# Kernel optimization log

Measured on AMD Instinct MI355X. Metric: run time of the kernel, lower is better.

The kernel has to match this reference:

```python
import jax, jax.numpy as jnp
import numpy as np

D = 128          # node_state_dim
N_NODES = 5000
WINDOW = 10
N_TOTAL = WINDOW * N_NODES
E = 131072       # structural (int) edges
T = 2            # message passing steps
HID = 1024


def setup_inputs() -> dict:
    key = jax.random.key(0)
    ks = jax.random.split(key, 20)
    ie = jax.random.randint(ks[0], (E, 3), 0, N_NODES, dtype=jnp.int32)
    int_edges = jnp.stack([ie[:, 0] % WINDOW, ie[:, 1], ie[:, 2]], axis=1)
    nodes = jax.random.randint(ks[1], (N_NODES,), 0, 10, dtype=jnp.int32)

    def init(k, shape, scale=0.05):
        return (jax.random.normal(k, shape, jnp.float32) * scale)

    params = dict(
        embed_table=init(ks[2], (10, D)),
        msg_W1=init(ks[3], (2 * D, HID)), msg_b1=jnp.zeros((HID,), jnp.float32),
        msg_W2=init(ks[4], (HID, D)), msg_b2=jnp.zeros((D,), jnp.float32),
        gru_int_W=init(ks[5], (D, 3 * D)), gru_int_U=init(ks[6], (D, 3 * D)),
        gru_int_b=jnp.zeros((2, 3 * D), jnp.float32),
        gru_temp_W=init(ks[7], (D, 3 * D)), gru_temp_U=init(ks[8], (D, 3 * D)),
        gru_temp_b=jnp.zeros((2, 3 * D), jnp.float32),
        ro_W1=init(ks[9], (D, HID)), ro_b1=jnp.zeros((HID,), jnp.float32),
        ro_W2=init(ks[10], (HID, 512)), ro_b2=jnp.zeros((512,), jnp.float32),
        ro_W3=init(ks[11], (512, 10)), ro_b3=jnp.zeros((10,), jnp.float32),
    )
    return {"int_edges": int_edges, "nodes": nodes, **params}


def _temp_edges():
    fwd_src = np.arange(0, N_TOTAL - N_NODES)
    fwd_dst = fwd_src + N_NODES
    bwd_src = np.arange(N_NODES, N_TOTAL)
    bwd_dst = bwd_src - N_NODES
    src = jnp.asarray(np.concatenate([fwd_src, bwd_src]), jnp.int32)
    dst = jnp.asarray(np.concatenate([fwd_dst, bwd_dst]), jnp.int32)
    return src, dst


def _gru(x, h, W, U, b):
    # Keras GRUCell, reset_after=True. x,h: [N,D]; W,U: [D,3D]; b: [2,3D]
    xg = x @ W + b[0]
    hg = h @ U + b[1]
    xz, xr, xh = jnp.split(xg, 3, axis=-1)
    hz, hr, hh = jnp.split(hg, 3, axis=-1)
    z = jax.nn.sigmoid(xz + hz)
    r = jax.nn.sigmoid(xr + hr)
    hcand = jnp.tanh(xh + r * hh)
    return z * h + (1.0 - z) * hcand


def _msg(x, W1, b1, W2, b2):
    # Dense(1024,relu) -> Dropout(inference: identity) -> Dense(D,relu)
    return jax.nn.relu(jax.nn.relu(x @ W1 + b1) @ W2 + b2)


def _seg_mean(x, idx, n):
    s = jax.ops.segment_sum(x, idx, num_segments=n)
    c = jax.ops.segment_sum(jnp.ones((x.shape[0],), x.dtype), idx, num_segments=n)
    return jnp.where(c[:, None] > 0, s / jnp.maximum(c, 1.0)[:, None], 0.0)


def reference(int_edges, nodes, embed_table, msg_W1, msg_b1, msg_W2, msg_b2,
              gru_int_W, gru_int_U, gru_int_b, gru_temp_W, gru_temp_U, gru_temp_b,
              ro_W1, ro_b1, ro_W2, ro_b2, ro_W3, ro_b3):
    node_idx = int_edges[:, 0] * N_NODES + int_edges[:, 1]        # [E]
    neigh_idx = int_edges[:, 0] * N_NODES + int_edges[:, 2]       # [E]
    t_src, t_dst = _temp_edges()

    h = embed_table[nodes]                                        # [n_nodes, D]
    h = jnp.repeat(h, WINDOW, axis=0)                             # [N_TOTAL, D]

    for _ in range(T):
        # structural edges
        m_in = jnp.concatenate([h[node_idx], h[neigh_idx]], axis=1)   # [E, 2D]
        m = _msg(m_in, msg_W1, msg_b1, msg_W2, msg_b2)                # [E, D]
        agg = _seg_mean(m, neigh_idx, N_TOTAL)                        # [N_TOTAL, D]
        h = _gru(agg, h, gru_int_W, gru_int_U, gru_int_b)
        # temporal edges
        tm_in = jnp.concatenate([h[t_src], h[t_dst]], axis=1)
        tm = _msg(tm_in, msg_W1, msg_b1, msg_W2, msg_b2)
        tagg = _seg_mean(tm, t_dst, N_TOTAL)
        h = _gru(tagg, h, gru_temp_W, gru_temp_U, gru_temp_b)

    # readout on first frame's nodes
    x = h[:N_NODES]
    x = jax.nn.relu(x @ ro_W1 + ro_b1)
    x = jax.nn.relu(x @ ro_W2 + ro_b2)
    return jax.nn.softmax(x @ ro_W3 + ro_b3, axis=-1)
```

## Files before the change

kernel.cpp:

```cpp
#include <hip/hip_runtime.h>
#include <math.h>

#define D 128
#define N_NODES 5000
#define WINDOW 10
#define N_TOTAL 50000
#define NE_INT 131072
#define NE_TMP 90000
#define NE_FWD (N_TOTAL - N_NODES)
#define HID 1024

typedef short bf16x8 __attribute__((ext_vector_type(8)));
typedef float f32x4 __attribute__((ext_vector_type(4)));

#define SA 264
#define SH 136
#define SK 136
#define SCAN_B 256

static __device__ __forceinline__ short f2bf(float f) {
    union { float f; unsigned u; } v; v.f = f;
    unsigned r = v.u + 0x7fffu + ((v.u >> 16) & 1u);
    return (short)(r >> 16);
}
static __device__ __forceinline__ float bf2f(short s) {
    union { unsigned u; float f; } v;
    v.u = ((unsigned)(unsigned short)s) << 16;
    return v.f;
}
static __device__ __forceinline__ float lo_bf(unsigned u) {
    union { unsigned u; float f; } v; v.u = u << 16; return v.f;
}
static __device__ __forceinline__ float hi_bf(unsigned u) {
    union { unsigned u; float f; } v; v.u = u & 0xffff0000u; return v.f;
}

struct TcvtArgs {
    const float* in[8];
    short* out[8];
    int K[8];
    int N[8];
};
__global__ void k_tcvt8(TcvtArgs a) {
    int i = blockIdx.x * blockDim.x + threadIdx.x;
#pragma unroll
    for (int s = 0; s < 8; ++s) {
        int sz = a.K[s] * a.N[s];
        if (i < sz) {
            int n = i / a.K[s], k = i - n * a.K[s];
            a.out[s][i] = f2bf(a.in[s][(size_t)k * a.N[s] + n]);
            return;
        }
        i -= sz;
    }
}

__global__ void k_init_h(const int* __restrict__ nodes, const float* __restrict__ embed,
                         float* __restrict__ h32, short* __restrict__ h16) {
    int i = blockIdx.x * blockDim.x + threadIdx.x;
    if (i >= N_TOTAL * D) return;
    int row = i >> 7;
    int c = i & 127;
    int n = nodes[row / WINDOW];
    float v = embed[n * D + c];
    h32[i] = v;
    h16[i] = f2bf(v);
}

__global__ void k_build_int_edges(const int* __restrict__ ie, int* __restrict__ src,
                                  int* __restrict__ dst, int* __restrict__ icnt) {
    int e = blockIdx.x * blockDim.x + threadIdx.x;
    if (e >= NE_INT) return;
    int t = ie[e * 3 + 0], a = ie[e * 3 + 1], b = ie[e * 3 + 2];
    int d = t * N_NODES + b;
    src[e] = t * N_NODES + a;
    dst[e] = d;
    atomicAdd(&icnt[d], 1);
}

__global__ void k_build_tmp_edges(int* __restrict__ src, int* __restrict__ dst) {
    int e = blockIdx.x * blockDim.x + threadIdx.x;
    if (e >= NE_TMP) return;
    int s, d;
    if (e < NE_FWD) { s = e; d = e + N_NODES; }
    else { int q = e - NE_FWD; s = q + N_NODES; d = q; }
    src[e] = s;
    dst[e] = d;
}

__global__ void k_scan_partial(const int* __restrict__ cnt, int* __restrict__ rowstart,
                               int* __restrict__ btot, int n) {
    __shared__ int s[SCAN_B];
    int tid = threadIdx.x;
    int i = blockIdx.x * SCAN_B + tid;
    int v = (i < n) ? cnt[i] : 0;
    s[tid] = v;
    __syncthreads();
    for (int off = 1; off < SCAN_B; off <<= 1) {
        int x = (tid >= off) ? s[tid - off] : 0;
        __syncthreads();
        s[tid] += x;
        __syncthreads();
    }
    if (i < n) rowstart[i] = s[tid] - v;
    if (tid == SCAN_B - 1) btot[blockIdx.x] = s[tid];
}

__global__ void k_scan_block(int* __restrict__ btot, int nb) {
    __shared__ int s[SCAN_B];
    int tid = threadIdx.x;
    int v = (tid < nb) ? btot[tid] : 0;
    s[tid] = v;
    __syncthreads();
    for (int off = 1; off < SCAN_B; off <<= 1) {
        int x = (tid >= off) ? s[tid - off] : 0;
        __syncthreads();
        s[tid] += x;
        __syncthreads();
    }
    if (tid < nb) btot[tid] = s[tid] - v;
}

__global__ void k_scan_add(int* __restrict__ rowstart, const int* __restrict__ btot,
                           int* __restrict__ cursor, int n, int total) {
    int i = blockIdx.x * blockDim.x + threadIdx.x;
    if (i < n) {
        int v = rowstart[i] + btot[i >> 8];
        rowstart[i] = v;
        cursor[i] = v;
    }
    if (i == 0) rowstart[n] = total;
}

__global__ void k_fill_csr(const int* __restrict__ dst, int nE, int* __restrict__ cursor,
                           int* __restrict__ pmap) {
    int e = blockIdx.x * blockDim.x + threadIdx.x;
    if (e >= nE) return;
    int p = atomicAdd(&cursor[dst[e]], 1);
    pmap[e] = p;
}

__global__ void __launch_bounds__(256, 1) k_msg_mfma(
    const short* __restrict__ h16, const int* __restrict__ src, const int* __restrict__ dst,
    const int* __restrict__ pmap, int nE,
    const short* __restrict__ W1T, const float* __restrict__ b1,
    const short* __restrict__ W2T, const float* __restrict__ b2,
    short* __restrict__ m)
{
    __shared__ short Ain[128 * SA];
    __shared__ short Hid[128 * SH];

    int t = threadIdx.x;
    int e0 = blockIdx.x * 128;

    {
        int r = t >> 1, q = t & 1;
        int e = e0 + r;
        int ec = (e < nE) ? e : (nE - 1);
        uint4* ao = (uint4*)(Ain + r * SA);
        if (q == 0) {
            const uint4* ps = (const uint4*)(h16 + (size_t)src[ec] * D);
#pragma unroll
            for (int i = 0; i < 16; ++i) ao[i] = ps[i];
        } else {
            const uint4* pd = (const uint4*)(h16 + (size_t)dst[ec] * D);
#pragma unroll
            for (int i = 0; i < 16; ++i) ao[16 + i] = pd[i];
        }
    }
    __syncthreads();

    int w = t >> 6, lane = t & 63;
    int lm = lane & 15, lk = lane >> 4;

    f32x4 c2[2][8];
#pragma unroll
    for (int cs = 0; cs < 2; ++cs) {
        int out0 = w * 32 + cs * 16 + lk * 4;
#pragma unroll
        for (int et = 0; et < 8; ++et)
#pragma unroll
            for (int rg = 0; rg < 4; ++rg) c2[cs][et][rg] = b2[out0 + rg];
    }

    for (int hc = 0; hc < 8; ++hc) {
        f32x4 c1[2][8];
#pragma unroll
        for (int cs = 0; cs < 2; ++cs) {
            int ch0 = hc * 128 + w * 32 + cs * 16 + lk * 4;
#pragma unroll
            for (int et = 0; et < 8; ++et)
#pragma unroll
                for (int rg = 0; rg < 4; ++rg) c1[cs][et][rg] = b1[ch0 + rg];
        }
#pragma unroll
        for (int kk = 0; kk < 8; ++kk) {
            int ko = kk * 32 + lk * 8;
            bf16x8 a0 = *(const bf16x8*)(W1T + (size_t)(hc * 128 + w * 32 + lm) * 256 + ko);
            bf16x8 a1 = *(const bf16x8*)(W1T + (size_t)(hc * 128 + w * 32 + 16 + lm) * 256 + ko);
            bf16x8 bf[8];
#pragma unroll
            for (int et = 0; et < 8; ++et)
                bf[et] = *(const bf16x8*)(Ain + (et * 16 + lm) * SA + ko);
#pragma unroll
            for (int et = 0; et < 8; ++et) {
                c1[0][et] = __builtin_amdgcn_mfma_f32_16x16x32_bf16(a0, bf[et], c1[0][et], 0, 0, 0);
                c1[1][et] = __builtin_amdgcn_mfma_f32_16x16x32_bf16(a1, bf[et], c1[1][et], 0, 0, 0);
            }
        }
        __syncthreads();
#pragma unroll
        for (int cs = 0; cs < 2; ++cs) {
            int ch_in = w * 32 + cs * 16 + lk * 4;
#pragma unroll
            for (int et = 0; et < 8; ++et) {
                int edge = et * 16 + lm;
                short4 sv;
                sv.x = f2bf(fmaxf(c1[cs][et][0], 0.f));
                sv.y = f2bf(fmaxf(c1[cs][et][1], 0.f));
                sv.z = f2bf(fmaxf(c1[cs][et][2], 0.f));
                sv.w = f2bf(fmaxf(c1[cs][et][3], 0.f));
                *(short4*)(Hid + edge * SH + ch_in) = sv;
            }
        }
        __syncthreads();

#pragma unroll
        for (int kk = 0; kk < 4; ++kk) {
            int ko = kk * 32 + lk * 8;
            bf16x8 a0 = *(const bf16x8*)(W2T + (size_t)(w * 32 + lm) * 1024 + hc * 128 + ko);
            bf16x8 a1 = *(const bf16x8*)(W2T + (size_t)(w * 32 + 16 + lm) * 1024 + hc * 128 + ko);
            bf16x8 bf[8];
#pragma unroll
            for (int et = 0; et < 8; ++et)
                bf[et] = *(const bf16x8*)(Hid + (et * 16 + lm) * SH + ko);
#pragma unroll
            for (int et = 0; et < 8; ++et) {
                c2[0][et] = __builtin_amdgcn_mfma_f32_16x16x32_bf16(a0, bf[et], c2[0][et], 0, 0, 0);
                c2[1][et] = __builtin_amdgcn_mfma_f32_16x16x32_bf16(a1, bf[et], c2[1][et], 0, 0, 0);
            }
        }
    }

#pragma unroll
    for (int et = 0; et < 8; ++et) {
        int edge = et * 16 + lm;
        int e = e0 + edge;
        if (e >= nE) continue;
        int slot = pmap ? pmap[e] : e;
        short* rowp = m + (size_t)slot * 128;
#pragma unroll
        for (int cs = 0; cs < 2; ++cs) {
            int out0 = w * 32 + cs * 16 + lk * 4;
            short4 sv;
            sv.x = f2bf(fmaxf(c2[cs][et][0], 0.f));
            sv.y = f2bf(fmaxf(c2[cs][et][1], 0.f));
            sv.z = f2bf(fmaxf(c2[cs][et][2], 0.f));
            sv.w = f2bf(fmaxf(c2[cs][et][3], 0.f));
            *(short4*)(rowp + out0) = sv;
        }
    }
}

__global__ void __launch_bounds__(256, 4) k_gru_mfma(
    const short* __restrict__ m, const int* __restrict__ rowstart, int mode,
    float* __restrict__ h32, short* __restrict__ h16,
    const short* __restrict__ WT, const short* __restrict__ UT,
    const float* __restrict__ b)
{
    __shared__ short Ax[64 * SK];
    __shared__ short Hx[64 * SK];
    int t = threadIdx.x;
    int r0 = blockIdx.x * 64;

    {
        int r = t >> 2, q = t & 3;
        int row = r0 + r;
        int rc = (row < N_TOTAL) ? row : (N_TOTAL - 1);
        const uint4* hp = (const uint4*)(h16 + (size_t)rc * D);
        uint4* hxo = (uint4*)(Hx + r * SK);
#pragma unroll
        for (int i = 0; i < 4; ++i) hxo[q * 4 + i] = hp[q * 4 + i];

        float acc[32];
#pragma unroll
        for (int i = 0; i < 32; ++i) acc[i] = 0.f;
        int deg = 0;
        if (row < N_TOTAL) {
            if (mode == 0) {
                int s0 = rowstart[row], s1 = rowstart[row + 1];
                deg = s1 - s0;
                for (int p = s0; p < s1; ++p) {
                    const uint4* mp = (const uint4*)(m + (size_t)p * 128 + q * 32);
#pragma unroll
                    for (int i = 0; i < 4; ++i) {
                        uint4 v = mp[i];
                        unsigned ua[4] = {v.x, v.y, v.z, v.w};
#pragma unroll
                        for (int j = 0; j < 4; ++j) {
                            acc[i * 8 + 2 * j]     += lo_bf(ua[j]);
                            acc[i * 8 + 2 * j + 1] += hi_bf(ua[j]);
                        }
                    }
                }
            } else {
                if (row >= N_NODES) {
                    const uint4* mp = (const uint4*)(m + (size_t)(row - N_NODES) * 128 + q * 32);
                    ++deg;
#pragma unroll
                    for (int i = 0; i < 4; ++i) {
                        uint4 v = mp[i];
                        unsigned ua[4] = {v.x, v.y, v.z, v.w};
#pragma unroll
                        for (int j = 0; j < 4; ++j) {
                            acc[i * 8 + 2 * j]     += lo_bf(ua[j]);
                            acc[i * 8 + 2 * j + 1] += hi_bf(ua[j]);
                        }
                    }
                }
                if (row < NE_FWD) {
                    const uint4* mp = (const uint4*)(m + (size_t)(NE_FWD + row) * 128 + q * 32);
                    ++deg;
#pragma unroll
                    for (int i = 0; i < 4; ++i) {
                        uint4 v = mp[i];
                        unsigned ua[4] = {v.x, v.y, v.z, v.w};
#pragma unroll
                        for (int j = 0; j < 4; ++j) {
                            acc[i * 8 + 2 * j]     += lo_bf(ua[j]);
                            acc[i * 8 + 2 * j + 1] += hi_bf(ua[j]);
                        }
                    }
                }
            }
        }
        float inv = (deg > 0) ? 1.f / (float)deg : 0.f;
        uint4* axp = (uint4*)(Ax + r * SK + q * 32);
#pragma unroll
        for (int i = 0; i < 4; ++i) {
            union { uint4 u; short s[8]; } pk;
#pragma unroll
            for (int j = 0; j < 8; ++j) pk.s[j] = f2bf(acc[i * 8 + j] * inv);
            axp[i] = pk.u;
        }
    }
    __syncthreads();

    int w = t >> 6, lane = t & 63;
    int lm = lane & 15, lk = lane >> 4;

    for (int g = 0; g < 8; ++g) {
        int ch = g * 16 + lm;
        f32x4 cxz, cxr, cxh, chz, chr_, chh;
#pragma unroll
        for (int rg = 0; rg < 4; ++rg) {
            cxz[rg] = b[ch];        chz[rg] = b[384 + ch];
            cxr[rg] = b[128 + ch];  chr_[rg] = b[384 + 128 + ch];
            cxh[rg] = b[256 + ch];  chh[rg] = b[384 + 256 + ch];
        }
#pragma unroll
        for (int kk = 0; kk < 4; ++kk) {
            int ko = kk * 32 + lk * 8;
            bf16x8 ax = *(const bf16x8*)(Ax + (w * 16 + lm) * SK + ko);
            bf16x8 hx = *(const bf16x8*)(Hx + (w * 16 + lm) * SK + ko);
            bf16x8 bz = *(const bf16x8*)(WT + (size_t)(ch) * 128 + ko);
            bf16x8 br = *(const bf16x8*)(WT + (size_t)(128 + ch) * 128 + ko);
            bf16x8 bh = *(const bf16x8*)(WT + (size_t)(256 + ch) * 128 + ko);
            bf16x8 uz = *(const bf16x8*)(UT + (size_t)(ch) * 128 + ko);
            bf16x8 ur = *(const bf16x8*)(UT + (size_t)(128 + ch) * 128 + ko);
            bf16x8 uh = *(const bf16x8*)(UT + (size_t)(256 + ch) * 128 + ko);
            cxz = __builtin_amdgcn_mfma_f32_16x16x32_bf16(ax, bz, cxz, 0, 0, 0);
            cxr = __builtin_amdgcn_mfma_f32_16x16x32_bf16(ax, br, cxr, 0, 0, 0);
            cxh = __builtin_amdgcn_mfma_f32_16x16x32_bf16(ax, bh, cxh, 0, 0, 0);
            chz = __builtin_amdgcn_mfma_f32_16x16x32_bf16(hx, uz, chz, 0, 0, 0);
            chr_ = __builtin_amdgcn_mfma_f32_16x16x32_bf16(hx, ur, chr_, 0, 0, 0);
            chh = __builtin_amdgcn_mfma_f32_16x16x32_bf16(hx, uh, chh, 0, 0, 0);
        }
#pragma unroll
        for (int rg = 0; rg < 4; ++rg) {
            int row = r0 + w * 16 + lk * 4 + rg;
            if (row >= N_TOTAL) continue;
            float z = 1.f / (1.f + expf(-(cxz[rg] + chz[rg])));
            float r_ = 1.f / (1.f + expf(-(cxr[rg] + chr_[rg])));
            float hcv = tanhf(cxh[rg] + r_ * chh[rg]);
            size_t idx = (size_t)row * D + ch;
            float hold = h32[idx];
            float hnew = z * hold + (1.f - z) * hcv;
            h32[idx] = hnew;
            h16[idx] = f2bf(hnew);
        }
    }
}

__global__ void __launch_bounds__(256, 4) k_ro_mfma(
    const short* __restrict__ A16, const short* __restrict__ BT,
    const float* __restrict__ bias, float* __restrict__ C32, short* __restrict__ C16,
    int M, int N, int K)
{
    __shared__ short As[64 * SK];
    int t = threadIdx.x;
    int mb = blockIdx.y * 64;
    int nb = blockIdx.x * 128;
    int w = t >> 6, lane = t & 63;
    int lm = lane & 15, lk = lane >> 4;

    f32x4 acc[8];
#pragma unroll
    for (int nt = 0; nt < 8; ++nt) {
        float bv = bias[nb + nt * 16 + lm];
        acc[nt][0] = bv; acc[nt][1] = bv; acc[nt][2] = bv; acc[nt][3] = bv;
    }

    for (int kc = 0; kc < K; kc += 128) {
        __syncthreads();
        {
            int r = t >> 2, q = t & 3;
            int row = mb + r;
            int rc = (row < M) ? row : (M - 1);
            const uint4* ap = (const uint4*)(A16 + (size_t)rc * K + kc);
            uint4* ao = (uint4*)(As + r * SK);
#pragma unroll
            for (int i = 0; i < 4; ++i) ao[i * 4 + q] = ap[i * 4 + q];
        }
        __syncthreads();
#pragma unroll
        for (int kk = 0; kk < 4; ++kk) {
            int ko = kk * 32 + lk * 8;
            bf16x8 a = *(const bf16x8*)(As + (w * 16 + lm) * SK + ko);
#pragma unroll
            for (int nt = 0; nt < 8; ++nt) {
                bf16x8 bfr = *(const bf16x8*)(BT + (size_t)(nb + nt * 16 + lm) * K + kc + ko);
                acc[nt] = __builtin_amdgcn_mfma_f32_16x16x32_bf16(a, bfr, acc[nt], 0, 0, 0);
            }
        }
    }
#pragma unroll
    for (int nt = 0; nt < 8; ++nt) {
        int col = nb + nt * 16 + lm;
#pragma unroll
        for (int rg = 0; rg < 4; ++rg) {
            int row = mb + w * 16 + lk * 4 + rg;
            if (row >= M) continue;
            float v = fmaxf(acc[nt][rg], 0.f);
            if (C32) C32[(size_t)row * N + col] = v;
            if (C16) C16[(size_t)row * N + col] = f2bf(v);
        }
    }
}

__global__ void __launch_bounds__(64) k_logits_softmax(
    const float* __restrict__ r2, const float* __restrict__ W3,
    const float* __restrict__ b3, float* __restrict__ out)
{
    int row = blockIdx.x;
    int t = threadIdx.x;
    float p[10];
#pragma unroll
    for (int j = 0; j < 10; ++j) p[j] = 0.f;
    for (int k = t; k < 512; k += 64) {
        float v = r2[(size_t)row * 512 + k];
#pragma unroll
        for (int j = 0; j < 10; ++j) p[j] += v * W3[k * 10 + j];
    }
#pragma unroll
    for (int j = 0; j < 10; ++j) {
        float s = p[j];
        for (int off = 32; off > 0; off >>= 1) s += __shfl_down(s, off);
        p[j] = s;
    }
    if (t == 0) {
        float mx = -1e30f;
#pragma unroll
        for (int j = 0; j < 10; ++j) { p[j] += b3[j]; mx = fmaxf(mx, p[j]); }
        float sum = 0.f;
#pragma unroll
        for (int j = 0; j < 10; ++j) { p[j] = expf(p[j] - mx); sum += p[j]; }
        float inv = 1.f / sum;
#pragma unroll
        for (int j = 0; j < 10; ++j) out[(size_t)row * 10 + j] = p[j] * inv;
    }
}

extern "C" void kernel_launch(void* const* d_in, const int* in_sizes, int n_in,
                              void* d_out, int out_size, void* d_ws, size_t ws_size,
                              hipStream_t stream)
{
    const int*   ie    = (const int*)d_in[0];
    const int*   nodes = (const int*)d_in[1];
    const float* embed = (const float*)d_in[2];
    const float* mW1   = (const float*)d_in[3];
    const float* mb1   = (const float*)d_in[4];
    const float* mW2   = (const float*)d_in[5];
    const float* mb2   = (const float*)d_in[6];
    const float* giW   = (const float*)d_in[7];
    const float* giU   = (const float*)d_in[8];
    const float* gib   = (const float*)d_in[9];
    const float* gtW   = (const float*)d_in[10];
    const float* gtU   = (const float*)d_in[11];
    const float* gtb   = (const float*)d_in[12];
    const float* rW1   = (const float*)d_in[13];
    const float* rb1   = (const float*)d_in[14];
    const float* rW2   = (const float*)d_in[15];
    const float* rb2   = (const float*)d_in[16];
    const float* rW3   = (const float*)d_in[17];
    const float* rb3   = (const float*)d_in[18];
    float* out = (float*)d_out;

    char* ws = (char*)d_ws;
    size_t off = 0;
    auto alloc = [&](size_t bytes) {
        void* p = ws + off;
        off += (bytes + 255) & ~(size_t)255;
        return p;
    };
    float* h32   = (float*)alloc((size_t)N_TOTAL * D * 4);
    short* h16   = (short*)alloc((size_t)N_TOTAL * D * 2);
    short* m     = (short*)alloc((size_t)NE_INT * 128 * 2);
    int*   icnt  = (int*)alloc((size_t)N_TOTAL * 4);
    int*   rowst = (int*)alloc((size_t)(N_TOTAL + 1) * 4);
    int*   btot  = (int*)alloc(256 * 4);
    int*   curs  = (int*)alloc((size_t)N_TOTAL * 4);
    int*   pmap  = (int*)alloc((size_t)NE_INT * 4);
    int*   srcA  = (int*)alloc((size_t)NE_INT * 4);
    int*   dstA  = (int*)alloc((size_t)NE_INT * 4);
    int*   srcT  = (int*)alloc((size_t)NE_TMP * 4);
    int*   dstT  = (int*)alloc((size_t)NE_TMP * 4);
    short* mW1T  = (short*)alloc((size_t)HID * 256 * 2);
    short* mW2T  = (short*)alloc((size_t)D * HID * 2);
    short* giWT  = (short*)alloc((size_t)384 * D * 2);
    short* giUT  = (short*)alloc((size_t)384 * D * 2);
    short* gtWT  = (short*)alloc((size_t)384 * D * 2);
    short* gtUT  = (short*)alloc((size_t)384 * D * 2);
    short* rW1T  = (short*)alloc((size_t)HID * D * 2);
    short* rW2T  = (short*)alloc((size_t)512 * HID * 2);
    short* r1_16 = (short*)alloc((size_t)N_NODES * HID * 2);
    float* r2_32 = (float*)alloc((size_t)N_NODES * 512 * 4);

    {
        TcvtArgs a;
        a.in[0] = mW1; a.out[0] = mW1T; a.K[0] = 256; a.N[0] = HID;
        a.in[1] = mW2; a.out[1] = mW2T; a.K[1] = HID; a.N[1] = D;
        a.in[2] = giW; a.out[2] = giWT; a.K[2] = D;   a.N[2] = 384;
        a.in[3] = giU; a.out[3] = giUT; a.K[3] = D;   a.N[3] = 384;
        a.in[4] = gtW; a.out[4] = gtWT; a.K[4] = D;   a.N[4] = 384;
        a.in[5] = gtU; a.out[5] = gtUT; a.K[5] = D;   a.N[5] = 384;
        a.in[6] = rW1; a.out[6] = rW1T; a.K[6] = D;   a.N[6] = HID;
        a.in[7] = rW2; a.out[7] = rW2T; a.K[7] = HID; a.N[7] = 512;
        int total = 256 * HID + HID * D + 4 * (D * 384) + D * HID + HID * 512;
        k_tcvt8<<<(total + 255) / 256, 256, 0, stream>>>(a);
    }

    hipMemsetAsync(icnt, 0, (size_t)N_TOTAL * 4, stream);
    k_init_h<<<(N_TOTAL * D + 255) / 256, 256, 0, stream>>>(nodes, embed, h32, h16);
    k_build_int_edges<<<(NE_INT + 255) / 256, 256, 0, stream>>>(ie, srcA, dstA, icnt);
    k_build_tmp_edges<<<(NE_TMP + 255) / 256, 256, 0, stream>>>(srcT, dstT);
    int nb = (N_TOTAL + SCAN_B - 1) / SCAN_B;
    k_scan_partial<<<nb, SCAN_B, 0, stream>>>(icnt, rowst, btot, N_TOTAL);
    k_scan_block<<<1, SCAN_B, 0, stream>>>(btot, nb);
    k_scan_add<<<nb, SCAN_B, 0, stream>>>(rowst, btot, curs, N_TOTAL, NE_INT);
    k_fill_csr<<<(NE_INT + 255) / 256, 256, 0, stream>>>(dstA, NE_INT, curs, pmap);

    int gmsgA = (NE_INT + 127) / 128;
    int gmsgT = (NE_TMP + 127) / 128;
    int ggru = (N_TOTAL + 63) / 64;
    for (int it = 0; it < 2; ++it) {
        k_msg_mfma<<<gmsgA, 256, 0, stream>>>(h16, srcA, dstA, pmap, NE_INT, mW1T, mb1, mW2T, mb2, m);
        k_gru_mfma<<<ggru, 256, 0, stream>>>(m, rowst, 0, h32, h16, giWT, giUT, gib);

        k_msg_mfma<<<gmsgT, 256, 0, stream>>>(h16, srcT, dstT, (const int*)nullptr, NE_TMP, mW1T, mb1, mW2T, mb2, m);
        k_gru_mfma<<<ggru, 256, 0, stream>>>(m, rowst, 1, h32, h16, gtWT, gtUT, gtb);
    }

    dim3 g1(HID / 128, (N_NODES + 63) / 64);
    k_ro_mfma<<<g1, 256, 0, stream>>>(h16, rW1T, rb1, (float*)nullptr, r1_16, N_NODES, HID, D);
    dim3 g2(512 / 128, (N_NODES + 63) / 64);
    k_ro_mfma<<<g2, 256, 0, stream>>>(r1_16, rW2T, rb2, r2_32, (short*)nullptr, N_NODES, 512, HID);
    k_logits_softmax<<<N_NODES, 64, 0, stream>>>(r2_32, rW3, rb3, out);
}
```

Measured before the change: 1.240 ms.

## Fuse segment-mean scatter into message kernel via fp32 atomics, drop CSR build

The message kernel now atomically adds each ReLU'd fp32 message into a per-node aggregation buffer indexed by destination. Previously it wrote bf16 messages into CSR slots and the GRU kernel gathered them. This removes the scan and CSR-fill kernels and the gather loop in the GRU, and avoids materializing per-edge messages. The cost is 128 fp32 atomics per edge, a memset of the 25.6MB aggregation buffer before each message pass, and summation order that is no longer deterministic.

```diff
diff --git a/kernel.cpp b/kernel.cpp
--- a/kernel.cpp
+++ b/kernel.cpp
@@ -16,7 +16,6 @@
 #define SA 264
 #define SH 136
 #define SK 136
-#define SCAN_B 256
 
 static __device__ __forceinline__ short f2bf(float f) {
     union { float f; unsigned u; } v; v.f = f;
@@ -27,12 +26,6 @@
     union { unsigned u; float f; } v;
     v.u = ((unsigned)(unsigned short)s) << 16;
     return v.f;
-}
-static __device__ __forceinline__ float lo_bf(unsigned u) {
-    union { unsigned u; float f; } v; v.u = u << 16; return v.f;
-}
-static __device__ __forceinline__ float hi_bf(unsigned u) {
-    union { unsigned u; float f; } v; v.u = u & 0xffff0000u; return v.f;
 }
 
 struct TcvtArgs {
@@ -88,64 +81,12 @@
     dst[e] = d;
 }
 
-__global__ void k_scan_partial(const int* __restrict__ cnt, int* __restrict__ rowstart,
-                               int* __restrict__ btot, int n) {
-    __shared__ int s[SCAN_B];
-    int tid = threadIdx.x;
-    int i = blockIdx.x * SCAN_B + tid;
-    int v = (i < n) ? cnt[i] : 0;
-    s[tid] = v;
-    __syncthreads();
-    for (int off = 1; off < SCAN_B; off <<= 1) {
-        int x = (tid >= off) ? s[tid - off] : 0;
-        __syncthreads();
-        s[tid] += x;
-        __syncthreads();
-    }
-    if (i < n) rowstart[i] = s[tid] - v;
-    if (tid == SCAN_B - 1) btot[blockIdx.x] = s[tid];
-}
-
-__global__ void k_scan_block(int* __restrict__ btot, int nb) {
-    __shared__ int s[SCAN_B];
-    int tid = threadIdx.x;
-    int v = (tid < nb) ? btot[tid] : 0;
-    s[tid] = v;
-    __syncthreads();
-    for (int off = 1; off < SCAN_B; off <<= 1) {
-        int x = (tid >= off) ? s[tid - off] : 0;
-        __syncthreads();
-        s[tid] += x;
-        __syncthreads();
-    }
-    if (tid < nb) btot[tid] = s[tid] - v;
-}
-
-__global__ void k_scan_add(int* __restrict__ rowstart, const int* __restrict__ btot,
-                           int* __restrict__ cursor, int n, int total) {
-    int i = blockIdx.x * blockDim.x + threadIdx.x;
-    if (i < n) {
-        int v = rowstart[i] + btot[i >> 8];
-        rowstart[i] = v;
-        cursor[i] = v;
-    }
-    if (i == 0) rowstart[n] = total;
-}
-
-__global__ void k_fill_csr(const int* __restrict__ dst, int nE, int* __restrict__ cursor,
-                           int* __restrict__ pmap) {
-    int e = blockIdx.x * blockDim.x + threadIdx.x;
-    if (e >= nE) return;
-    int p = atomicAdd(&cursor[dst[e]], 1);
-    pmap[e] = p;
-}
-
 __global__ void __launch_bounds__(256, 1) k_msg_mfma(
     const short* __restrict__ h16, const int* __restrict__ src, const int* __restrict__ dst,
-    const int* __restrict__ pmap, int nE,
+    int nE,
     const short* __restrict__ W1T, const float* __restrict__ b1,
     const short* __restrict__ W2T, const float* __restrict__ b2,
-    short* __restrict__ m)
+    float* __restrict__ agg)
 {
     __shared__ short Ain[128 * SA];
     __shared__ short Hid[128 * SH];
@@ -247,23 +188,20 @@
         int edge = et * 16 + lm;
         int e = e0 + edge;
         if (e >= nE) continue;
-        int slot = pmap ? pmap[e] : e;
-        short* rowp = m + (size_t)slot * 128;
+        int d = dst[e];
+        float* rowp = agg + (size_t)d * 128;
 #pragma unroll
         for (int cs = 0; cs < 2; ++cs) {
             int out0 = w * 32 + cs * 16 + lk * 4;
-            short4 sv;
-            sv.x = f2bf(fmaxf(c2[cs][et][0], 0.f));
-            sv.y = f2bf(fmaxf(c2[cs][et][1], 0.f));
-            sv.z = f2bf(fmaxf(c2[cs][et][2], 0.f));
-            sv.w = f2bf(fmaxf(c2[cs][et][3], 0.f));
-            *(short4*)(rowp + out0) = sv;
+#pragma unroll
+            for (int rg = 0; rg < 4; ++rg)
+                atomicAdd(rowp + out0 + rg, fmaxf(c2[cs][et][rg], 0.f));
         }
     }
 }
 
 __global__ void __launch_bounds__(256, 4) k_gru_mfma(
-    const short* __restrict__ m, const int* __restrict__ rowstart, int mode,
+    const float* __restrict__ agg, const int* __restrict__ icnt, int mode,
     float* __restrict__ h32, short* __restrict__ h16,
     const short* __restrict__ WT, const short* __restrict__ UT,
     const float* __restrict__ b)
@@ -282,65 +220,20 @@
 #pragma unroll
         for (int i = 0; i < 4; ++i) hxo[q * 4 + i] = hp[q * 4 + i];
 
-        float acc[32];
-#pragma unroll
-        for (int i = 0; i < 32; ++i) acc[i] = 0.f;
-        int deg = 0;
-        if (row < N_TOTAL) {
-            if (mode == 0) {
-                int s0 = rowstart[row], s1 = rowstart[row + 1];
-                deg = s1 - s0;
-                for (int p = s0; p < s1; ++p) {
-                    const uint4* mp = (const uint4*)(m + (size_t)p * 128 + q * 32);
-#pragma unroll
-                    for (int i = 0; i < 4; ++i) {
-                        uint4 v = mp[i];
-                        unsigned ua[4] = {v.x, v.y, v.z, v.w};
-#pragma unroll
-                        for (int j = 0; j < 4; ++j) {
-                            acc[i * 8 + 2 * j]     += lo_bf(ua[j]);
-                            acc[i * 8 + 2 * j + 1] += hi_bf(ua[j]);
-                        }
-                    }
-                }
-            } else {
-                if (row >= N_NODES) {
-                    const uint4* mp = (const uint4*)(m + (size_t)(row - N_NODES) * 128 + q * 32);
-                    ++deg;
-#pragma unroll
-                    for (int i = 0; i < 4; ++i) {
-                        uint4 v = mp[i];
-                        unsigned ua[4] = {v.x, v.y, v.z, v.w};
-#pragma unroll
-                        for (int j = 0; j < 4; ++j) {
-                            acc[i * 8 + 2 * j]     += lo_bf(ua[j]);
-                            acc[i * 8 + 2 * j + 1] += hi_bf(ua[j]);
-                        }
-                    }
-                }
-                if (row < NE_FWD) {
-                    const uint4* mp = (const uint4*)(m + (size_t)(NE_FWD + row) * 128 + q * 32);
-                    ++deg;
-#pragma unroll
-                    for (int i = 0; i < 4; ++i) {
-                        uint4 v = mp[i];
-                        unsigned ua[4] = {v.x, v.y, v.z, v.w};
-#pragma unroll
-                        for (int j = 0; j < 4; ++j) {
-                            acc[i * 8 + 2 * j]     += lo_bf(ua[j]);
-                            acc[i * 8 + 2 * j + 1] += hi_bf(ua[j]);
-                        }
-                    }
-                }
-            }
+        int deg;
+        if (mode == 0) {
+            deg = icnt[rc];
+        } else {
+            deg = (rc >= N_NODES ? 1 : 0) + (rc < NE_FWD ? 1 : 0);
         }
         float inv = (deg > 0) ? 1.f / (float)deg : 0.f;
+        const float* ap = agg + (size_t)rc * 128 + q * 32;
         uint4* axp = (uint4*)(Ax + r * SK + q * 32);
 #pragma unroll
         for (int i = 0; i < 4; ++i) {
             union { uint4 u; short s[8]; } pk;
 #pragma unroll
-            for (int j = 0; j < 8; ++j) pk.s[j] = f2bf(acc[i * 8 + j] * inv);
+            for (int j = 0; j < 8; ++j) pk.s[j] = f2bf(ap[i * 8 + j] * inv);
             axp[i] = pk.u;
         }
     }
@@ -515,12 +408,8 @@
     };
     float* h32   = (float*)alloc((size_t)N_TOTAL * D * 4);
     short* h16   = (short*)alloc((size_t)N_TOTAL * D * 2);
-    short* m     = (short*)alloc((size_t)NE_INT * 128 * 2);
+    float* agg   = (float*)alloc((size_t)N_TOTAL * D * 4);
     int*   icnt  = (int*)alloc((size_t)N_TOTAL * 4);
-    int*   rowst = (int*)alloc((size_t)(N_TOTAL + 1) * 4);
-    int*   btot  = (int*)alloc(256 * 4);
-    int*   curs  = (int*)alloc((size_t)N_TOTAL * 4);
-    int*   pmap  = (int*)alloc((size_t)NE_INT * 4);
     int*   srcA  = (int*)alloc((size_t)NE_INT * 4);
     int*   dstA  = (int*)alloc((size_t)NE_INT * 4);
     int*   srcT  = (int*)alloc((size_t)NE_TMP * 4);
@@ -554,21 +443,19 @@
     k_init_h<<<(N_TOTAL * D + 255) / 256, 256, 0, stream>>>(nodes, embed, h32, h16);
     k_build_int_edges<<<(NE_INT + 255) / 256, 256, 0, stream>>>(ie, srcA, dstA, icnt);
     k_build_tmp_edges<<<(NE_TMP + 255) / 256, 256, 0, stream>>>(srcT, dstT);
-    int nb = (N_TOTAL + SCAN_B - 1) / SCAN_B;
-    k_scan_partial<<<nb, SCAN_B, 0, stream>>>(icnt, rowst, btot, N_TOTAL);
-    k_scan_block<<<1, SCAN_B, 0, stream>>>(btot, nb);
-    k_scan_add<<<nb, SCAN_B, 0, stream>>>(rowst, btot, curs, N_TOTAL, NE_INT);
-    k_fill_csr<<<(NE_INT + 255) / 256, 256, 0, stream>>>(dstA, NE_INT, curs, pmap);
 
     int gmsgA = (NE_INT + 127) / 128;
     int gmsgT = (NE_TMP + 127) / 128;
     int ggru = (N_TOTAL + 63) / 64;
+    size_t aggB = (size_t)N_TOTAL * D * 4;
     for (int it = 0; it < 2; ++it) {
-        k_msg_mfma<<<gmsgA, 256, 0, stream>>>(h16, srcA, dstA, pmap, NE_INT, mW1T, mb1, mW2T, mb2, m);
-        k_gru_mfma<<<ggru, 256, 0, stream>>>(m, rowst, 0, h32, h16, giWT, giUT, gib);
-
-        k_msg_mfma<<<gmsgT, 256, 0, stream>>>(h16, srcT, dstT, (const int*)nullptr, NE_TMP, mW1T, mb1, mW2T, mb2, m);
-        k_gru_mfma<<<ggru, 256, 0, stream>>>(m, rowst, 1, h32, h16, gtWT, gtUT, gtb);
+        hipMemsetAsync(agg, 0, aggB, stream);
+        k_msg_mfma<<<gmsgA, 256, 0, stream>>>(h16, srcA, dstA, NE_INT, mW1T, mb1, mW2T, mb2, agg);
+        k_gru_mfma<<<ggru, 256, 0, stream>>>(agg, icnt, 0, h32, h16, giWT, giUT, gib);
+
+        hipMemsetAsync(agg, 0, aggB, stream);
+        k_msg_mfma<<<gmsgT, 256, 0, stream>>>(h16, srcT, dstT, NE_TMP, mW1T, mb1, mW2T, mb2, agg);
+        k_gru_mfma<<<ggru, 256, 0, stream>>>(agg, icnt, 1, h32, h16, gtWT, gtUT, gtb);
     }
 
     dim3 g1(HID / 128, (N_NODES + 63) / 64);
```

Measured after the change: 1.765 ms. +42.3%, slower.

## Fuse temporal-edge message MLP, mean aggregation and GRU into one persistent kernel

Applied to the files above, without the earlier changes.

Replaces the temporal-edge message kernel and its GRU kernel with one persistent kernel. The kernel derives the fixed forward and backward temporal neighbours of each 64-row group directly, runs the two-layer message MLP for both edge directions, averages them in LDS and applies the GRU with MFMA. This removes the write and read-back of the temporal message buffer, the edge-index arrays and a launch per step. To avoid read/write races it ping-pongs h16 into a second buffer that aliases the readout scratch (r1_16, spilling into r2_32). The cost is one block per CU due to the large LDS footprint, plus MLP work on masked boundary edges.

```diff
diff --git a/kernel.cpp b/kernel.cpp
--- a/kernel.cpp
+++ b/kernel.cpp
@@ -78,16 +78,6 @@
     atomicAdd(&icnt[d], 1);
 }
 
-__global__ void k_build_tmp_edges(int* __restrict__ src, int* __restrict__ dst) {
-    int e = blockIdx.x * blockDim.x + threadIdx.x;
-    if (e >= NE_TMP) return;
-    int s, d;
-    if (e < NE_FWD) { s = e; d = e + N_NODES; }
-    else { int q = e - NE_FWD; s = q + N_NODES; d = q; }
-    src[e] = s;
-    dst[e] = d;
-}
-
 __global__ void k_scan_partial(const int* __restrict__ cnt, int* __restrict__ rowstart,
                                int* __restrict__ btot, int n) {
     __shared__ int s[SCAN_B];
@@ -224,7 +214,6 @@
             }
         }
         __syncthreads();
-
 #pragma unroll
         for (int kk = 0; kk < 4; ++kk) {
             int ko = kk * 32 + lk * 8;
@@ -262,8 +251,182 @@
     }
 }
 
+__global__ void __launch_bounds__(256, 1) k_tmp_fused(
+    const short* __restrict__ hin, float* __restrict__ h32, short* __restrict__ hout,
+    const short* __restrict__ W1T, const float* __restrict__ b1,
+    const short* __restrict__ W2T, const float* __restrict__ b2,
+    const short* __restrict__ WT, const short* __restrict__ UT,
+    const float* __restrict__ gb)
+{
+    __shared__ short Ain[128 * SA];
+    __shared__ short Hid[128 * SH];
+
+    int t = threadIdx.x;
+    int w = t >> 6, lane = t & 63;
+    int lm = lane & 15, lk = lane >> 4;
+    const int NG = (N_TOTAL + 63) / 64;
+
+    for (int grp = blockIdx.x; grp < NG; grp += gridDim.x) {
+        int r0 = grp * 64;
+        __syncthreads();
+
+        {
+            int s = t >> 1, q = t & 1;
+            int j = s & 63;
+            int rc = r0 + j; if (rc >= N_TOTAL) rc = N_TOTAL - 1;
+            int srcrow;
+            if (s < 64) srcrow = (rc >= N_NODES) ? rc - N_NODES : rc;
+            else        srcrow = (rc < NE_FWD) ? rc + N_NODES : rc;
+            uint4* ao = (uint4*)(Ain + s * SA);
+            if (q == 0) {
+                const uint4* ps = (const uint4*)(hin + (size_t)srcrow * D);
+#pragma unroll
+                for (int i = 0; i < 16; ++i) ao[i] = ps[i];
+            } else {
+                const uint4* pd = (const uint4*)(hin + (size_t)rc * D);
+#pragma unroll
+                for (int i = 0; i < 16; ++i) ao[16 + i] = pd[i];
+            }
+        }
+        __syncthreads();
+
+        f32x4 c2[2][8];
+#pragma unroll
+        for (int cs = 0; cs < 2; ++cs) {
+            int out0 = w * 32 + cs * 16 + lk * 4;
+#pragma unroll
+            for (int et = 0; et < 8; ++et)
+#pragma unroll
+                for (int rg = 0; rg < 4; ++rg) c2[cs][et][rg] = b2[out0 + rg];
+        }
+        for (int hc = 0; hc < 8; ++hc) {
+            f32x4 c1[2][8];
+#pragma unroll
+            for (int cs = 0; cs < 2; ++cs) {
+                int ch0 = hc * 128 + w * 32 + cs * 16 + lk * 4;
+#pragma unroll
+                for (int et = 0; et < 8; ++et)
+#pragma unroll
+                    for (int rg = 0; rg < 4; ++rg) c1[cs][et][rg] = b1[ch0 + rg];
+            }
+#pragma unroll
+            for (int kk = 0; kk < 8; ++kk) {
+                int ko = kk * 32 + lk * 8;
+                bf16x8 a0 = *(const bf16x8*)(W1T + (size_t)(hc * 128 + w * 32 + lm) * 256 + ko);
+                bf16x8 a1 = *(const bf16x8*)(W1T + (size_t)(hc * 128 + w * 32 + 16 + lm) * 256 + ko);
+                bf16x8 bf[8];
+#pragma unroll
+                for (int et = 0; et < 8; ++et)
+                    bf[et] = *(const bf16x8*)(Ain + (et * 16 + lm) * SA + ko);
+#pragma unroll
+                for (int et = 0; et < 8; ++et) {
+                    c1[0][et] = __builtin_amdgcn_mfma_f32_16x16x32_bf16(a0, bf[et], c1[0][et], 0, 0, 0);
+                    c1[1][et] = __builtin_amdgcn_mfma_f32_16x16x32_bf16(a1, bf[et], c1[1][et], 0, 0, 0);
+                }
+            }
+            __syncthreads();
+#pragma unroll
+            for (int cs = 0; cs < 2; ++cs) {
+                int ch_in = w * 32 + cs * 16 + lk * 4;
+#pragma unroll
+                for (int et = 0; et < 8; ++et) {
+                    int edge = et * 16 + lm;
+                    short4 sv;
+                    sv.x = f2bf(fmaxf(c1[cs][et][0], 0.f));
+                    sv.y = f2bf(fmaxf(c1[cs][et][1], 0.f));
+                    sv.z = f2bf(fmaxf(c1[cs][et][2], 0.f));
+                    sv.w = f2bf(fmaxf(c1[cs][et][3], 0.f));
+                    *(short4*)(Hid + edge * SH + ch_in) = sv;
+                }
+            }
+            __syncthreads();
+#pragma unroll
+            for (int kk = 0; kk < 4; ++kk) {
+                int ko = kk * 32 + lk * 8;
+                bf16x8 a0 = *(const bf16x8*)(W2T + (size_t)(w * 32 + lm) * 1024 + hc * 128 + ko);
+                bf16x8 a1 = *(const bf16x8*)(W2T + (size_t)(w * 32 + 16 + lm) * 1024 + hc * 128 + ko);
+                bf16x8 bf[8];
+#pragma unroll
+                for (int et = 0; et < 8; ++et)
+                    bf[et] = *(const bf16x8*)(Hid + (et * 16 + lm) * SH + ko);
+#pragma unroll
+                for (int et = 0; et < 8; ++et) {
+                    c2[0][et] = __builtin_amdgcn_mfma_f32_16x16x32_bf16(a0, bf[et], c2[0][et], 0, 0, 0);
+                    c2[1][et] = __builtin_amdgcn_mfma_f32_16x16x32_bf16(a1, bf[et], c2[1][et], 0, 0, 0);
+                }
+            }
+        }
+
+        __syncthreads();
+#pragma unroll
+        for (int cs = 0; cs < 2; ++cs) {
+            int out0 = w * 32 + cs * 16 + lk * 4;
+#pragma unroll
+            for (int et = 0; et < 4; ++et) {
+                int j = et * 16 + lm;
+                int r = r0 + j;
+                float fv = (r >= N_NODES) ? 1.f : 0.f;
+                float bv = (r < NE_FWD) ? 1.f : 0.f;
+                float inv = 1.f / fmaxf(fv + bv, 1.f);
+                short4 sv;
+#pragma unroll
+                for (int rg = 0; rg < 4; ++rg) {
+                    float mf = fmaxf(c2[cs][et][rg], 0.f);
+                    float mb = fmaxf(c2[cs][et + 4][rg], 0.f);
+                    float v = (fv * mf + bv * mb) * inv;
+                    ((short*)&sv)[rg] = f2bf(v);
+                }
+                *(short4*)(Hid + j * SH + out0) = sv;
+            }
+        }
+        __syncthreads();
+
+        for (int g = 0; g < 8; ++g) {
+            int ch = g * 16 + lm;
+            f32x4 cxz, cxr, cxh, chz, chr_, chh;
+#pragma unroll
+            for (int rg = 0; rg < 4; ++rg) {
+                cxz[rg] = gb[ch];        chz[rg] = gb[384 + ch];
+                cxr[rg] = gb[128 + ch];  chr_[rg] = gb[384 + 128 + ch];
+                cxh[rg] = gb[256 + ch];  chh[rg] = gb[384 + 256 + ch];
+            }
+#pragma unroll
+            for (int kk = 0; kk < 4; ++kk) {
+                int ko = kk * 32 + lk * 8;
+                bf16x8 ax = *(const bf16x8*)(Hid + (w * 16 + lm) * SH + ko);
+                bf16x8 hx = *(const bf16x8*)(Ain + (w * 16 + lm) * SA + 128 + ko);
+                bf16x8 bz = *(const bf16x8*)(WT + (size_t)(ch) * 128 + ko);
+                bf16x8 br = *(const bf16x8*)(WT + (size_t)(128 + ch) * 128 + ko);
+                bf16x8 bh = *(const bf16x8*)(WT + (size_t)(256 + ch) * 128 + ko);
+                bf16x8 uz = *(const bf16x8*)(UT + (size_t)(ch) * 128 + ko);
+                bf16x8 ur = *(const bf16x8*)(UT + (size_t)(128 + ch) * 128 + ko);
+                bf16x8 uh = *(const bf16x8*)(UT + (size_t)(256 + ch) * 128 + ko);
+                cxz = __builtin_amdgcn_mfma_f32_16x16x32_bf16(ax, bz, cxz, 0, 0, 0);
+                cxr = __builtin_amdgcn_mfma_f32_16x16x32_bf16(ax, br, cxr, 0, 0, 0);
+                cxh = __builtin_amdgcn_mfma_f32_16x16x32_bf16(ax, bh, cxh, 0, 0, 0);
+                chz = __builtin_amdgcn_mfma_f32_16x16x32_bf16(hx, uz, chz, 0, 0, 0);
+                chr_ = __builtin_amdgcn_mfma_f32_16x16x32_bf16(hx, ur, chr_, 0, 0, 0);
+                chh = __builtin_amdgcn_mfma_f32_16x16x32_bf16(hx, uh, chh, 0, 0, 0);
+            }
+#pragma unroll
+            for (int rg = 0; rg < 4; ++rg) {
+                int row = r0 + w * 16 + lk * 4 + rg;
+                if (row >= N_TOTAL) continue;
+                float z = 1.f / (1.f + expf(-(cxz[rg] + chz[rg])));
+                float r_ = 1.f / (1.f + expf(-(cxr[rg] + chr_[rg])));
+                float hcv = tanhf(cxh[rg] + r_ * chh[rg]);
+                size_t idx = (size_t)row * D + ch;
+                float hold = h32[idx];
+                float hnew = z * hold + (1.f - z) * hcv;
+                h32[idx] = hnew;
+                hout[idx] = f2bf(hnew);
+            }
+        }
+    }
+}
+
 __global__ void __launch_bounds__(256, 4) k_gru_mfma(
-    const short* __restrict__ m, const int* __restrict__ rowstart, int mode,
+    const short* __restrict__ m, const int* __restrict__ rowstart,
     float* __restrict__ h32, short* __restrict__ h16,
     const short* __restrict__ WT, const short* __restrict__ UT,
     const float* __restrict__ b)
@@ -287,49 +450,18 @@
         for (int i = 0; i < 32; ++i) acc[i] = 0.f;
         int deg = 0;
         if (row < N_TOTAL) {
-            if (mode == 0) {
-                int s0 = rowstart[row], s1 = rowstart[row + 1];
-                deg = s1 - s0;
-                for (int p = s0; p < s1; ++p) {
-                    const uint4* mp = (const uint4*)(m + (size_t)p * 128 + q * 32);
-#pragma unroll
-                    for (int i = 0; i < 4; ++i) {
-                        uint4 v = mp[i];
-                        unsigned ua[4] = {v.x, v.y, v.z, v.w};
-#pragma unroll
-                        for (int j = 0; j < 4; ++j) {
-                            acc[i * 8 + 2 * j]     += lo_bf(ua[j]);
-                            acc[i * 8 + 2 * j + 1] += hi_bf(ua[j]);
-                        }
-                    }
-                }
-            } else {
-                if (row >= N_NODES) {
-                    const uint4* mp = (const uint4*)(m + (size_t)(row - N_NODES) * 128 + q * 32);
-                    ++deg;
-#pragma unroll
-                    for (int i = 0; i < 4; ++i) {
-                        uint4 v = mp[i];
-                        unsigned ua[4] = {v.x, v.y, v.z, v.w};
-#pragma unroll
-                        for (int j = 0; j < 4; ++j) {
-                            acc[i * 8 + 2 * j]     += lo_bf(ua[j]);
-                            acc[i * 8 + 2 * j + 1] += hi_bf(ua[j]);
-                        }
-                    }
-                }
-                if (row < NE_FWD) {
-                    const uint4* mp = (const uint4*)(m + (size_t)(NE_FWD + row) * 128 + q * 32);
-                    ++deg;
-#pragma unroll
-                    for (int i = 0; i < 4; ++i) {
-                        uint4 v = mp[i];
-                        unsigned ua[4] = {v.x, v.y, v.z, v.w};
-#pragma unroll
-                        for (int j = 0; j < 4; ++j) {
-                            acc[i * 8 + 2 * j]     += lo_bf(ua[j]);
-                            acc[i * 8 + 2 * j + 1] += hi_bf(ua[j]);
-                        }
+            int s0 = rowstart[row], s1 = rowstart[row + 1];
+            deg = s1 - s0;
+            for (int p = s0; p < s1; ++p) {
+                const uint4* mp = (const uint4*)(m + (size_t)p * 128 + q * 32);
+#pragma unroll
+                for (int i = 0; i < 4; ++i) {
+                    uint4 v = mp[i];
+                    unsigned ua[4] = {v.x, v.y, v.z, v.w};
+#pragma unroll
+                    for (int j = 0; j < 4; ++j) {
+                        acc[i * 8 + 2 * j]     += lo_bf(ua[j]);
+                        acc[i * 8 + 2 * j + 1] += hi_bf(ua[j]);
                     }
                 }
             }
@@ -514,7 +646,7 @@
         return p;
     };
     float* h32   = (float*)alloc((size_t)N_TOTAL * D * 4);
-    short* h16   = (short*)alloc((size_t)N_TOTAL * D * 2);
+    short* h16a  = (short*)alloc((size_t)N_TOTAL * D * 2);
     short* m     = (short*)alloc((size_t)NE_INT * 128 * 2);
     int*   icnt  = (int*)alloc((size_t)N_TOTAL * 4);
     int*   rowst = (int*)alloc((size_t)(N_TOTAL + 1) * 4);
@@ -523,8 +655,6 @@
     int*   pmap  = (int*)alloc((size_t)NE_INT * 4);
     int*   srcA  = (int*)alloc((size_t)NE_INT * 4);
     int*   dstA  = (int*)alloc((size_t)NE_INT * 4);
-    int*   srcT  = (int*)alloc((size_t)NE_TMP * 4);
-    int*   dstT  = (int*)alloc((size_t)NE_TMP * 4);
     short* mW1T  = (short*)alloc((size_t)HID * 256 * 2);
     short* mW2T  = (short*)alloc((size_t)D * HID * 2);
     short* giWT  = (short*)alloc((size_t)384 * D * 2);
@@ -535,6 +665,7 @@
     short* rW2T  = (short*)alloc((size_t)512 * HID * 2);
     short* r1_16 = (short*)alloc((size_t)N_NODES * HID * 2);
     float* r2_32 = (float*)alloc((size_t)N_NODES * 512 * 4);
+    short* h16b  = r1_16;
 
     {
         TcvtArgs a;
@@ -551,9 +682,8 @@
     }
 
     hipMemsetAsync(icnt, 0, (size_t)N_TOTAL * 4, stream);
-    k_init_h<<<(N_TOTAL * D + 255) / 256, 256, 0, stream>>>(nodes, embed, h32, h16);
+    k_init_h<<<(N_TOTAL * D + 255) / 256, 256, 0, stream>>>(nodes, embed, h32, h16a);
     k_build_int_edges<<<(NE_INT + 255) / 256, 256, 0, stream>>>(ie, srcA, dstA, icnt);
-    k_build_tmp_edges<<<(NE_TMP + 255) / 256, 256, 0, stream>>>(srcT, dstT);
     int nb = (N_TOTAL + SCAN_B - 1) / SCAN_B;
     k_scan_partial<<<nb, SCAN_B, 0, stream>>>(icnt, rowst, btot, N_TOTAL);
     k_scan_block<<<1, SCAN_B, 0, stream>>>(btot, nb);
@@ -561,18 +691,20 @@
     k_fill_csr<<<(NE_INT + 255) / 256, 256, 0, stream>>>(dstA, NE_INT, curs, pmap);
 
     int gmsgA = (NE_INT + 127) / 128;
-    int gmsgT = (NE_TMP + 127) / 128;
     int ggru = (N_TOTAL + 63) / 64;
+    int gtmp = 768;
+    short* hc = h16a;
+    short* hn = h16b;
     for (int it = 0; it < 2; ++it) {
-        k_msg_mfma<<<gmsgA, 256, 0, stream>>>(h16, srcA, dstA, pmap, NE_INT, mW1T, mb1, mW2T, mb2, m);
-        k_gru_mfma<<<ggru, 256, 0, stream>>>(m, rowst, 0, h32, h16, giWT, giUT, gib);
-
-        k_msg_mfma<<<gmsgT, 256, 0, stream>>>(h16, srcT, dstT, (const int*)nullptr, NE_TMP, mW1T, mb1, mW2T, mb2, m);
-        k_gru_mfma<<<ggru, 256, 0, stream>>>(m, rowst, 1, h32, h16, gtWT, gtUT, gtb);
+        k_msg_mfma<<<gmsgA, 256, 0, stream>>>(hc, srcA, dstA, pmap, NE_INT, mW1T, mb1, mW2T, mb2, m);
+        k_gru_mfma<<<ggru, 256, 0, stream>>>(m, rowst, h32, hc, giWT, giUT, gib);
+
+        k_tmp_fused<<<gtmp, 256, 0, stream>>>(hc, h32, hn, mW1T, mb1, mW2T, mb2, gtWT, gtUT, gtb);
+        short* tmp = hc; hc = hn; hn = tmp;
     }
 
     dim3 g1(HID / 128, (N_NODES + 63) / 64);
-    k_ro_mfma<<<g1, 256, 0, stream>>>(h16, rW1T, rb1, (float*)nullptr, r1_16, N_NODES, HID, D);
+    k_ro_mfma<<<g1, 256, 0, stream>>>(hc, rW1T, rb1, (float*)nullptr, r1_16, N_NODES, HID, D);
     dim3 g2(512 / 128, (N_NODES + 63) / 64);
     k_ro_mfma<<<g2, 256, 0, stream>>>(r1_16, rW2T, rb2, r2_32, (short*)nullptr, N_NODES, 512, HID);
     k_logits_softmax<<<N_NODES, 64, 0, stream>>>(r2_32, rW3, rb3, out);
```

Result: slower. 1.322 ms (+6.6%).
